# Kernel tuning notes

Measured on AMD Instinct MI355X. Metric: run time of the kernel, lower is better.

## Reference

```python
import jax, jax.numpy as jnp
import numpy as np

EPS = 1e-5
B, CIN, L = 512, 5, 1024   # batch, input channels, msp length == d_model
COUT, A, NB = 32, 13, 5    # CNN branch channels, max_atoms, num_bonds_prediction


def conv1d(x, w, pad, groups=1):
    # x: (N, C, L), w: (O, I/groups, K)
    return jax.lax.conv_general_dilated(
        x, w, window_strides=(1,), padding=[(pad, pad)],
        dimension_numbers=("NCH", "OIH", "NCH"), feature_group_count=groups)


def batchnorm(x, g, b):
    # training-mode BN over (N, L) per channel, as nn.BatchNorm1d in train()
    m = jnp.mean(x, axis=(0, 2), keepdims=True)
    v = jnp.var(x, axis=(0, 2), keepdims=True)
    return (x - m) * jax.lax.rsqrt(v + EPS) * g[None, :, None] + b[None, :, None]


def setup_inputs() -> dict:
    key = jax.random.key(0)
    ks = jax.random.split(key, 16)
    n = jax.random.normal
    inp = {
        "src": n(ks[0], (B, CIN, L), dtype=jnp.float32),
        "mask": jnp.ones((B, A), dtype=bool),
        "max_atoms": A,
        # CNN branch 1 (kernel 5) : depthwise, pointwise, BN, residual 1x1 conv
        "dw1": n(ks[1], (CIN, 1, 5), dtype=jnp.float32) * 0.2,
        "pw1": n(ks[2], (COUT, CIN, 1), dtype=jnp.float32) * 0.2,
        "g1": jnp.ones((COUT,), jnp.float32),
        "be1": jnp.zeros((COUT,), jnp.float32),
        "r1w": n(ks[3], (COUT, CIN, 1), dtype=jnp.float32) * 0.2,
        "r1b": jnp.zeros((COUT,), jnp.float32),
        # CNN branch 2 (kernel 3)
        "dw2": n(ks[4], (CIN, 1, 3), dtype=jnp.float32) * 0.2,
        "pw2": n(ks[5], (COUT, CIN, 1), dtype=jnp.float32) * 0.2,
        "g2": jnp.ones((COUT,), jnp.float32),
        "be2": jnp.zeros((COUT,), jnp.float32),
        "r2w": n(ks[6], (COUT, CIN, 1), dtype=jnp.float32) * 0.2,
        "r2b": jnp.zeros((COUT,), jnp.float32),
        # EdgeClassify2 linears: ll1 (2*COUT -> A), fl (2*L -> NB)
        "ll1w": n(ks[7], (A, 2 * COUT), dtype=jnp.float32) * 0.1,
        "ll1b": jnp.zeros((A,), jnp.float32),
        "flw": n(ks[8], (NB, 2 * L), dtype=jnp.float32) * 0.02,
        "flb": jnp.zeros((NB,), jnp.float32),
    }
    return inp


def reference(src, mask, max_atoms, dw1, pw1, g1, be1, r1w, r1b,
              dw2, pw2, g2, be2, r2w, r2b, ll1w, ll1b, flw, flb):
    # ---- CNN encoder ----
    e1 = jax.nn.relu(batchnorm(conv1d(conv1d(src, dw1, 2, groups=CIN), pw1, 0), g1, be1))
    e1 = e1 * (conv1d(src, r1w, 0) + r1b[None, :, None])
    e2 = jax.nn.relu(batchnorm(conv1d(conv1d(src, dw2, 1, groups=CIN), pw2, 0), g2, be2))
    e2 = e2 * (conv1d(src, r2w, 0) + r2b[None, :, None])
    x = jnp.concatenate([e1, e2], axis=1)          # (B, 2*COUT, L)
    # ---- EdgeClassify2 ----
    # ll1 over channel dim: (B, 2*COUT, L) -> (B, A, L)
    h = jnp.einsum("bcl,ac->bal", x, ll1w) + ll1b[None, :, None]
    # vectorized replacement of the O(A^2) python loop:
    # final_e[:, i, j] = concat(h[:, min(i,j)], h[:, max(i,j)])
    idx = jnp.arange(max_atoms)
    mn = jnp.minimum(idx[:, None], idx[None, :])   # (A, A)
    mx = jnp.maximum(idx[:, None], idx[None, :])
    final_e = jnp.concatenate([h[:, mn, :], h[:, mx, :]], axis=-1)  # (B, A, A, 2L)
    out = jnp.einsum("bijd,nd->bijn", final_e, flw) + flb           # (B, A, A, NB)
    return out
```

## Files before the change

### kernel.cpp

```cpp
#include <hip/hip_runtime.h>
#include <hip/hip_bf16.h>

#define BB 512
#define LL 1024
#define AA 13
#define NBP 5
#define NTOT (BB * LL)
#define EPSV 1e-5f

#define WS_MOM   0
#define WS_F     192
#define WS_CONST 256

template<int CTRL, int RM, bool BC>
__device__ __forceinline__ float dppadd(float v) {
    int t = __builtin_amdgcn_update_dpp(0, __float_as_int(v), CTRL, RM, 0xf, BC);
    return v + __int_as_float(t);
}
__device__ __forceinline__ float wave_sum(float v) {
    v = dppadd<0x111, 0xf, true >(v);
    v = dppadd<0x112, 0xf, true >(v);
    v = dppadd<0x114, 0xf, true >(v);
    v = dppadd<0x118, 0xf, true >(v);
    v = dppadd<0x142, 0xa, false>(v);
    v = dppadd<0x143, 0xc, false>(v);
    return v;
}

__global__ __launch_bounds__(256) void k_moments(
    const float* __restrict__ src,
    const float* __restrict__ dw1,
    const float* __restrict__ dw2,
    const float* __restrict__ flw,
    float* __restrict__ ws)
{
    __shared__ float red[4][40];
    __shared__ float fred[4];
    int tid = threadIdx.x;
    int gid = blockIdx.x * 256 + tid;
    int b = gid >> 7, L0 = (gid & 127) << 3;
    const float* sb = src + b * (5 * LL);

    float w1[5][5], w2[5][3];
#pragma unroll
    for (int c = 0; c < 5; c++) {
#pragma unroll
        for (int t = 0; t < 5; t++) w1[c][t] = dw1[c*5+t];
#pragma unroll
        for (int t = 0; t < 3; t++) w2[c][t] = dw2[c*3+t];
    }

    float x[5][16];
#pragma unroll
    for (int c5 = 0; c5 < 5; c5++) {
        const float* sp = sb + c5 * LL;
        float4 xa = (L0 >= 4)     ? *(const float4*)(sp + L0 - 4) : make_float4(0,0,0,0);
        float4 xb = *(const float4*)(sp + L0);
        float4 xc = *(const float4*)(sp + L0 + 4);
        float4 xd = (L0 <= 1012)  ? *(const float4*)(sp + L0 + 8) : make_float4(0,0,0,0);
        x[c5][0]=xa.x; x[c5][1]=xa.y; x[c5][2]=xa.z; x[c5][3]=xa.w;
        x[c5][4]=xb.x; x[c5][5]=xb.y; x[c5][6]=xb.z; x[c5][7]=xb.w;
        x[c5][8]=xc.x; x[c5][9]=xc.y; x[c5][10]=xc.z; x[c5][11]=xc.w;
        x[c5][12]=xd.x; x[c5][13]=xd.y; x[c5][14]=xd.z; x[c5][15]=xd.w;
    }

    float acc[40];
#pragma unroll
    for (int k = 0; k < 40; k++) acc[k] = 0.f;

#pragma unroll
    for (int k = 0; k < 8; k++) {
        float d1[5], d2[5];
#pragma unroll
        for (int c5 = 0; c5 < 5; c5++) {
            d1[c5] = w1[c5][0]*x[c5][k+2] + w1[c5][1]*x[c5][k+3] + w1[c5][2]*x[c5][k+4]
                   + w1[c5][3]*x[c5][k+5] + w1[c5][4]*x[c5][k+6];
            d2[c5] = w2[c5][0]*x[c5][k+3] + w2[c5][1]*x[c5][k+4] + w2[c5][2]*x[c5][k+5];
        }
#pragma unroll
        for (int j = 0; j < 5; j++) { acc[j] += d1[j]; acc[20+j] += d2[j]; }
#pragma unroll
        for (int j = 0; j < 5; j++)
#pragma unroll
            for (int kk = j; kk < 5; kk++) {
                int idx = j*(11-j)/2 + (kk - j);
                acc[5+idx]  += d1[j]*d1[kk];
                acc[25+idx] += d2[j]*d2[kk];
            }
    }

    int lane = tid & 63, wv = tid >> 6;
#pragma unroll
    for (int k = 0; k < 40; k++) acc[k] = wave_sum(acc[k]);
    if (lane == 63) {
#pragma unroll
        for (int k = 0; k < 40; k++) red[wv][k] = acc[k];
    }
    __syncthreads();
    if (tid < 40) {
        float v = red[0][tid] + red[1][tid] + red[2][tid] + red[3][tid];
        atomicAdd(&ws[WS_MOM + tid], v);
    }

    if (blockIdx.x < 10) {
        int nn = blockIdx.x;
        int n = nn < 5 ? nn : nn - 5;
        int off = nn < 5 ? 0 : LL;
        float4 v = *(const float4*)(flw + n * (2*LL) + off + tid * 4);
        float s = wave_sum(v.x + v.y + v.z + v.w);
        if (lane == 63) fred[wv] = s;
        __syncthreads();
        if (tid == 0) ws[WS_F + nn] = fred[0] + fred[1] + fred[2] + fred[3];
    }
}

__global__ __launch_bounds__(64) void k_prep(
    float* __restrict__ ws,
    const float* __restrict__ pw1, const float* __restrict__ pw2,
    const float* __restrict__ g1,  const float* __restrict__ be1,
    const float* __restrict__ g2,  const float* __restrict__ be2,
    const float* __restrict__ r1w, const float* __restrict__ r2w,
    const float* __restrict__ r1b, const float* __restrict__ r2b)
{
    int t = threadIdx.x;
    int br = t >> 5, o = t & 31;
    const float invN = 1.0f / (float)NTOT;
    const float* pw = br ? pw2 : pw1;
    const float* rw = br ? r2w : r1w;
    const float* s  = ws + WS_MOM + (br ? 20 : 0);
    const float* M  = ws + WS_MOM + (br ? 25 : 5);
    float pwv[5], rwv[5], md[5];
#pragma unroll
    for (int j = 0; j < 5; j++) { pwv[j] = pw[o*5+j]; rwv[j] = rw[o*5+j]; md[j] = s[j] * invN; }
    float meanY = 0.f;
#pragma unroll
    for (int j = 0; j < 5; j++) meanY += pwv[j] * md[j];
    float ey2 = 0.f;
#pragma unroll
    for (int j = 0; j < 5; j++)
#pragma unroll
        for (int k = 0; k < 5; k++) {
            int lo = j < k ? j : k, hi = j < k ? k : j;
            int idx = lo*(11-lo)/2 + (hi - lo);
            ey2 += pwv[j] * pwv[k] * (M[idx] * invN);
        }
    float varY = ey2 - meanY * meanY;
    if (varY < 0.f) varY = 0.f;
    float gg = br ? g2[o] : g1[o];
    float bb = br ? be2[o] : be1[o];
    float rb = br ? r2b[o] : r1b[o];
    float sc = gg * rsqrtf(varY + EPSV);
    float sh = bb - meanY * sc;

    float* dst = ws + WS_CONST + t * 16;
    dst[0] = pwv[0]*sc; dst[1] = pwv[1]*sc; dst[2] = pwv[2]*sc; dst[3] = pwv[3]*sc;
    dst[4] = pwv[4]*sc; dst[5] = sh;        dst[6] = rb;        dst[7] = 0.f;
    dst[8] = rwv[0];    dst[9] = rwv[1];    dst[10] = rwv[2];   dst[11] = rwv[3];
    dst[12] = rwv[4];   dst[13] = 0.f;      dst[14] = 0.f;      dst[15] = 0.f;
}

__global__ __launch_bounds__(512) void k_fused(
    const float* __restrict__ src,
    const float* __restrict__ dw1,
    const float* __restrict__ dw2,
    const float* __restrict__ flw,
    const float* __restrict__ ll1w,
    const float* __restrict__ ll1b,
    const float* __restrict__ flb,
    const float* __restrict__ ws,
    float* __restrict__ out)
{
    __shared__ __align__(16) float srcS[5][1040];
    __shared__ __align__(16) float SLds[64][12];
    __shared__ float llT[832];
    __shared__ float PQ[130];

    int tid = threadIdx.x, b = blockIdx.x;
    int lane = tid & 63;
    int gu = __builtin_amdgcn_readfirstlane(tid >> 6);
    int br = gu >> 2;

    const float* srcB = src + b * (5 * LL);

    for (int idx = tid; idx < 5 * 256; idx += 512) {
        int c5 = idx >> 8, q = idx & 255;
        float4 v = *(const float4*)(srcB + (c5 << 10) + (q << 2));
        *(float4*)&srcS[c5][(q << 2) + 8] = v;
    }
    if (tid < 5)       { srcS[tid][6] = 0.f; srcS[tid][7] = 0.f; }
    else if (tid < 10) { srcS[tid-5][1032] = 0.f; srcS[tid-5][1033] = 0.f; }
    for (int idx = tid; idx < 832; idx += 512) {
        int cc = idx / 13, a = idx - cc * 13;
        llT[idx] = ll1w[a * 64 + cc];
    }
    __syncthreads();

    float wdw[5][5];
    if (br == 0) {
#pragma unroll
        for (int c5 = 0; c5 < 5; c5++)
#pragma unroll
            for (int t = 0; t < 5; t++) wdw[c5][t] = dw1[c5*5+t];
    } else {
#pragma unroll
        for (int c5 = 0; c5 < 5; c5++) {
            wdw[c5][0] = 0.f; wdw[c5][1] = dw2[c5*3+0];
            wdw[c5][2] = dw2[c5*3+1]; wdw[c5][3] = dw2[c5*3+2]; wdw[c5][4] = 0.f;
        }
    }
    const float* cb = ws + WS_CONST + gu * 128;

    float acc[80];
#pragma unroll
    for (int k = 0; k < 80; k++) acc[k] = 0.f;

#pragma unroll 1
    for (int p = 0; p < 4; p++) {
        int l0 = (p << 8) + (lane << 2);
        float4 fw[10];
#pragma unroll
        for (int nn = 0; nn < 10; nn++) {
            int n = nn < 5 ? nn : nn - 5;
            int off = nn < 5 ? 0 : LL;
            fw[nn] = *(const float4*)(flw + n * (2*LL) + off + l0);
        }
        float dv[5][4], sv[5][4];
#pragma unroll
        for (int c5 = 0; c5 < 5; c5++) {
            int i0 = l0 + 8;
            float2 lh = *(const float2*)&srcS[c5][i0 - 2];
            float4 ct = *(const float4*)&srcS[c5][i0];
            float2 rh = *(const float2*)&srcS[c5][i0 + 4];
            float xx[8] = {lh.x, lh.y, ct.x, ct.y, ct.z, ct.w, rh.x, rh.y};
            sv[c5][0] = ct.x; sv[c5][1] = ct.y; sv[c5][2] = ct.z; sv[c5][3] = ct.w;
#pragma unroll
            for (int q = 0; q < 4; q++)
                dv[c5][q] = wdw[c5][0]*xx[q]   + wdw[c5][1]*xx[q+1] + wdw[c5][2]*xx[q+2]
                          + wdw[c5][3]*xx[q+3] + wdw[c5][4]*xx[q+4];
        }
#pragma unroll
        for (int ci = 0; ci < 8; ci++) {
            const float4 A  = *(const float4*)(cb + ci*16);
            const float4 B2 = *(const float4*)(cb + ci*16 + 4);
            const float4 R0 = *(const float4*)(cb + ci*16 + 8);
            const float4 R1 = *(const float4*)(cb + ci*16 + 12);
#pragma unroll
            for (int q = 0; q < 4; q++) {
                float y = B2.y + A.x*dv[0][q] + A.y*dv[1][q] + A.z*dv[2][q]
                                + A.w*dv[3][q] + B2.x*dv[4][q];
                float r = B2.z + R0.x*sv[0][q] + R0.y*sv[1][q] + R0.z*sv[2][q]
                                + R0.w*sv[3][q] + R1.x*sv[4][q];
                float e = fmaxf(y, 0.f) * r;
#pragma unroll
                for (int nn = 0; nn < 10; nn++) {
                    float f = (nn==0)?fw[0].x:(nn==1)?fw[1].x:(nn==2)?fw[2].x:(nn==3)?fw[3].x:
                              (nn==4)?fw[4].x:(nn==5)?fw[5].x:(nn==6)?fw[6].x:(nn==7)?fw[7].x:
                              (nn==8)?fw[8].x:fw[9].x;
                    float fq = (q==0) ? f :
                               (q==1) ? ((nn==0)?fw[0].y:(nn==1)?fw[1].y:(nn==2)?fw[2].y:(nn==3)?fw[3].y:
                                         (nn==4)?fw[4].y:(nn==5)?fw[5].y:(nn==6)?fw[6].y:(nn==7)?fw[7].y:
                                         (nn==8)?fw[8].y:fw[9].y) :
                               (q==2) ? ((nn==0)?fw[0].z:(nn==1)?fw[1].z:(nn==2)?fw[2].z:(nn==3)?fw[3].z:
                                         (nn==4)?fw[4].z:(nn==5)?fw[5].z:(nn==6)?fw[6].z:(nn==7)?fw[7].z:
                                         (nn==8)?fw[8].z:fw[9].z) :
                                        ((nn==0)?fw[0].w:(nn==1)?fw[1].w:(nn==2)?fw[2].w:(nn==3)?fw[3].w:
                                         (nn==4)?fw[4].w:(nn==5)?fw[5].w:(nn==6)?fw[6].w:(nn==7)?fw[7].w:
                                         (nn==8)?fw[8].w:fw[9].w);
                    acc[ci*10 + nn] += e * fq;
                }
            }
        }
    }

#pragma unroll
    for (int k = 0; k < 80; k++) acc[k] = wave_sum(acc[k]);
    if (lane == 63) {
#pragma unroll
        for (int ci = 0; ci < 8; ci++) {
            int c = gu * 8 + ci;
            *(float4*)&SLds[c][0] = make_float4(acc[ci*10+0], acc[ci*10+1], acc[ci*10+2], acc[ci*10+3]);
            *(float4*)&SLds[c][4] = make_float4(acc[ci*10+4], acc[ci*10+5], acc[ci*10+6], acc[ci*10+7]);
            *(float2*)&SLds[c][8] = make_float2(acc[ci*10+8], acc[ci*10+9]);
        }
    }
    __syncthreads();

    if (tid < 130) {
        int half = tid >= 65 ? 1 : 0;
        int q = tid - half * 65;
        int a = q / 5, n = q - a * 5;
        int col = half * 5 + n;
        float v = ll1b[a] * ws[WS_F + col];
#pragma unroll 8
        for (int cc = 0; cc < 64; cc++) v += llT[cc * 13 + a] * SLds[cc][col];
        PQ[tid] = v;
    }
    __syncthreads();

    for (int idx = tid; idx < AA * AA * NBP; idx += 512) {
        int i = idx / 65;
        int rr = idx - i * 65;
        int j = rr / 5, n = rr - j * 5;
        int mn = i < j ? i : j, mx = i < j ? j : i;
        out[b * (AA * AA * NBP) + idx] = PQ[mn * 5 + n] + PQ[65 + mx * 5 + n] + flb[n];
    }
}

extern "C" void kernel_launch(void* const* d_in, const int* in_sizes, int n_in,
                              void* d_out, int out_size, void* d_ws, size_t ws_size,
                              hipStream_t stream) {
    const float* src  = (const float*)d_in[0];
    const float* dw1  = (const float*)d_in[3];
    const float* pw1  = (const float*)d_in[4];
    const float* g1   = (const float*)d_in[5];
    const float* be1  = (const float*)d_in[6];
    const float* r1w  = (const float*)d_in[7];
    const float* r1b  = (const float*)d_in[8];
    const float* dw2  = (const float*)d_in[9];
    const float* pw2  = (const float*)d_in[10];
    const float* g2   = (const float*)d_in[11];
    const float* be2  = (const float*)d_in[12];
    const float* r2w  = (const float*)d_in[13];
    const float* r2b  = (const float*)d_in[14];
    const float* ll1w = (const float*)d_in[15];
    const float* ll1b = (const float*)d_in[16];
    const float* flw  = (const float*)d_in[17];
    const float* flb  = (const float*)d_in[18];
    float* ws  = (float*)d_ws;
    float* out = (float*)d_out;

    hipMemsetAsync(d_ws, 0, 1024, stream);
    k_moments<<<256, 256, 0, stream>>>(src, dw1, dw2, flw, ws);
    k_prep<<<1, 64, 0, stream>>>(ws, pw1, pw2, g1, be1, g2, be2, r1w, r2w, r1b, r2b);
    k_fused<<<BB, 512, 0, stream>>>(src, dw1, dw2, flw, ll1w, ll1b, flb, ws, out);
}
```

Baseline: 155.3 us.

## Fold BN prep into fused kernel, drop memset and atomics via per-block partials

Replaces atomic accumulation of BN moments with per-block partial writes, removing the workspace memset. The single-block prep kernel is eliminated; every fused block reduces the 256 partials and computes BN/pointwise constants itself into LDS. Also restructures the inner accumulation to reduce the 4 positions before the 10 projection updates, splits the depthwise conv by branch to skip zero taps, and sets launch bounds to hint occupancy. Costs redundant per-block reduction of partials and extra LDS.

Result: slower. 482.1 us (+210.4%).

```diff
diff --git a/kernel.cpp b/kernel.cpp
--- a/kernel.cpp
+++ b/kernel.cpp
@@ -8,9 +8,8 @@
 #define NTOT (BB * LL)
 #define EPSV 1e-5f
 
-#define WS_MOM   0
-#define WS_F     192
-#define WS_CONST 256
+#define WS_F    192
+#define WS_PART 256
 
 template<int CTRL, int RM, bool BC>
 __device__ __forceinline__ float dppadd(float v) {
@@ -54,10 +53,10 @@
 #pragma unroll
     for (int c5 = 0; c5 < 5; c5++) {
         const float* sp = sb + c5 * LL;
-        float4 xa = (L0 >= 4)     ? *(const float4*)(sp + L0 - 4) : make_float4(0,0,0,0);
+        float4 xa = (L0 >= 4)    ? *(const float4*)(sp + L0 - 4) : make_float4(0,0,0,0);
         float4 xb = *(const float4*)(sp + L0);
         float4 xc = *(const float4*)(sp + L0 + 4);
-        float4 xd = (L0 <= 1012)  ? *(const float4*)(sp + L0 + 8) : make_float4(0,0,0,0);
+        float4 xd = (L0 <= 1012) ? *(const float4*)(sp + L0 + 8) : make_float4(0,0,0,0);
         x[c5][0]=xa.x; x[c5][1]=xa.y; x[c5][2]=xa.z; x[c5][3]=xa.w;
         x[c5][4]=xb.x; x[c5][5]=xb.y; x[c5][6]=xb.z; x[c5][7]=xb.w;
         x[c5][8]=xc.x; x[c5][9]=xc.y; x[c5][10]=xc.z; x[c5][11]=xc.w;
@@ -98,8 +97,8 @@
     }
     __syncthreads();
     if (tid < 40) {
-        float v = red[0][tid] + red[1][tid] + red[2][tid] + red[3][tid];
-        atomicAdd(&ws[WS_MOM + tid], v);
+        ws[WS_PART + blockIdx.x * 40 + tid] =
+            red[0][tid] + red[1][tid] + red[2][tid] + red[3][tid];
     }
 
     if (blockIdx.x < 10) {
@@ -114,55 +113,15 @@
     }
 }
 
-__global__ __launch_bounds__(64) void k_prep(
-    float* __restrict__ ws,
+__global__ __launch_bounds__(512, 4) void k_fused(
+    const float* __restrict__ src,
+    const float* __restrict__ dw1,
+    const float* __restrict__ dw2,
     const float* __restrict__ pw1, const float* __restrict__ pw2,
     const float* __restrict__ g1,  const float* __restrict__ be1,
     const float* __restrict__ g2,  const float* __restrict__ be2,
     const float* __restrict__ r1w, const float* __restrict__ r2w,
-    const float* __restrict__ r1b, const float* __restrict__ r2b)
-{
-    int t = threadIdx.x;
-    int br = t >> 5, o = t & 31;
-    const float invN = 1.0f / (float)NTOT;
-    const float* pw = br ? pw2 : pw1;
-    const float* rw = br ? r2w : r1w;
-    const float* s  = ws + WS_MOM + (br ? 20 : 0);
-    const float* M  = ws + WS_MOM + (br ? 25 : 5);
-    float pwv[5], rwv[5], md[5];
-#pragma unroll
-    for (int j = 0; j < 5; j++) { pwv[j] = pw[o*5+j]; rwv[j] = rw[o*5+j]; md[j] = s[j] * invN; }
-    float meanY = 0.f;
-#pragma unroll
-    for (int j = 0; j < 5; j++) meanY += pwv[j] * md[j];
-    float ey2 = 0.f;
-#pragma unroll
-    for (int j = 0; j < 5; j++)
-#pragma unroll
-        for (int k = 0; k < 5; k++) {
-            int lo = j < k ? j : k, hi = j < k ? k : j;
-            int idx = lo*(11-lo)/2 + (hi - lo);
-            ey2 += pwv[j] * pwv[k] * (M[idx] * invN);
-        }
-    float varY = ey2 - meanY * meanY;
-    if (varY < 0.f) varY = 0.f;
-    float gg = br ? g2[o] : g1[o];
-    float bb = br ? be2[o] : be1[o];
-    float rb = br ? r2b[o] : r1b[o];
-    float sc = gg * rsqrtf(varY + EPSV);
-    float sh = bb - meanY * sc;
-
-    float* dst = ws + WS_CONST + t * 16;
-    dst[0] = pwv[0]*sc; dst[1] = pwv[1]*sc; dst[2] = pwv[2]*sc; dst[3] = pwv[3]*sc;
-    dst[4] = pwv[4]*sc; dst[5] = sh;        dst[6] = rb;        dst[7] = 0.f;
-    dst[8] = rwv[0];    dst[9] = rwv[1];    dst[10] = rwv[2];   dst[11] = rwv[3];
-    dst[12] = rwv[4];   dst[13] = 0.f;      dst[14] = 0.f;      dst[15] = 0.f;
-}
-
-__global__ __launch_bounds__(512) void k_fused(
-    const float* __restrict__ src,
-    const float* __restrict__ dw1,
-    const float* __restrict__ dw2,
+    const float* __restrict__ r1b, const float* __restrict__ r2b,
     const float* __restrict__ flw,
     const float* __restrict__ ll1w,
     const float* __restrict__ ll1b,
@@ -171,7 +130,9 @@
     float* __restrict__ out)
 {
     __shared__ __align__(16) float srcS[5][1040];
+    __shared__ __align__(16) float constS[64][16];
     __shared__ __align__(16) float SLds[64][12];
+    __shared__ float momS[40];
     __shared__ float llT[832];
     __shared__ float PQ[130];
 
@@ -187,12 +148,61 @@
         float4 v = *(const float4*)(srcB + (c5 << 10) + (q << 2));
         *(float4*)&srcS[c5][(q << 2) + 8] = v;
     }
-    if (tid < 5)       { srcS[tid][6] = 0.f; srcS[tid][7] = 0.f; }
-    else if (tid < 10) { srcS[tid-5][1032] = 0.f; srcS[tid-5][1033] = 0.f; }
+    if (tid < 40) {
+        int c5 = tid >> 3, j = tid & 7;
+        int i = (j < 4) ? (4 + j) : (1028 + j);
+        srcS[c5][i] = 0.f;
+    }
     for (int idx = tid; idx < 832; idx += 512) {
         int cc = idx / 13, a = idx - cc * 13;
         llT[idx] = ll1w[a * 64 + cc];
     }
+    if (tid < 320) {
+        int k = tid >> 3, sub = tid & 7;
+        float v = 0.f;
+#pragma unroll 8
+        for (int t2 = 0; t2 < 32; t2++) v += ws[WS_PART + (sub + (t2 << 3)) * 40 + k];
+        v += __shfl_xor(v, 1, 64);
+        v += __shfl_xor(v, 2, 64);
+        v += __shfl_xor(v, 4, 64);
+        if (sub == 0) momS[k] = v;
+    }
+    __syncthreads();
+    if (tid < 64) {
+        int brc = tid >> 5, o = tid & 31;
+        const float invN = 1.0f / (float)NTOT;
+        const float* pw = brc ? pw2 : pw1;
+        const float* rw = brc ? r2w : r1w;
+        const float* s  = momS + (brc ? 20 : 0);
+        const float* M  = momS + (brc ? 25 : 5);
+        float pwv[5], rwv[5], md[5];
+#pragma unroll
+        for (int j = 0; j < 5; j++) { pwv[j] = pw[o*5+j]; rwv[j] = rw[o*5+j]; md[j] = s[j] * invN; }
+        float meanY = 0.f;
+#pragma unroll
+        for (int j = 0; j < 5; j++) meanY += pwv[j] * md[j];
+        float ey2 = 0.f;
+#pragma unroll
+        for (int j = 0; j < 5; j++)
+#pragma unroll
+            for (int k = 0; k < 5; k++) {
+                int lo = j < k ? j : k, hi = j < k ? k : j;
+                int idx = lo*(11-lo)/2 + (hi - lo);
+                ey2 += pwv[j] * pwv[k] * (M[idx] * invN);
+            }
+        float varY = ey2 - meanY * meanY;
+        if (varY < 0.f) varY = 0.f;
+        float gg = brc ? g2[o] : g1[o];
+        float bb = brc ? be2[o] : be1[o];
+        float rb = brc ? r2b[o] : r1b[o];
+        float sc = gg * rsqrtf(varY + EPSV);
+        float sh = bb - meanY * sc;
+        float* dst = &constS[tid][0];
+        dst[0] = pwv[0]*sc; dst[1] = pwv[1]*sc; dst[2] = pwv[2]*sc; dst[3] = pwv[3]*sc;
+        dst[4] = pwv[4]*sc; dst[5] = sh;        dst[6] = rb;        dst[7] = 0.f;
+        dst[8] = rwv[0];    dst[9] = rwv[1];    dst[10] = rwv[2];   dst[11] = rwv[3];
+        dst[12] = rwv[4];   dst[13] = 0.f;      dst[14] = 0.f;      dst[15] = 0.f;
+    }
     __syncthreads();
 
     float wdw[5][5];
@@ -204,70 +214,67 @@
     } else {
 #pragma unroll
         for (int c5 = 0; c5 < 5; c5++) {
-            wdw[c5][0] = 0.f; wdw[c5][1] = dw2[c5*3+0];
-            wdw[c5][2] = dw2[c5*3+1]; wdw[c5][3] = dw2[c5*3+2]; wdw[c5][4] = 0.f;
-        }
-    }
-    const float* cb = ws + WS_CONST + gu * 128;
+            wdw[c5][0] = 0.f;
+            wdw[c5][1] = dw2[c5*3+0]; wdw[c5][2] = dw2[c5*3+1]; wdw[c5][3] = dw2[c5*3+2];
+            wdw[c5][4] = 0.f;
+        }
+    }
 
     float acc[80];
 #pragma unroll
     for (int k = 0; k < 80; k++) acc[k] = 0.f;
+    int c0 = gu << 3;
 
 #pragma unroll 1
     for (int p = 0; p < 4; p++) {
         int l0 = (p << 8) + (lane << 2);
-        float4 fw[10];
+        float fwv[10][4];
 #pragma unroll
         for (int nn = 0; nn < 10; nn++) {
             int n = nn < 5 ? nn : nn - 5;
             int off = nn < 5 ? 0 : LL;
-            fw[nn] = *(const float4*)(flw + n * (2*LL) + off + l0);
+            float4 t4 = *(const float4*)(flw + n * (2*LL) + off + l0);
+            fwv[nn][0] = t4.x; fwv[nn][1] = t4.y; fwv[nn][2] = t4.z; fwv[nn][3] = t4.w;
         }
         float dv[5][4], sv[5][4];
 #pragma unroll
         for (int c5 = 0; c5 < 5; c5++) {
             int i0 = l0 + 8;
-            float2 lh = *(const float2*)&srcS[c5][i0 - 2];
-            float4 ct = *(const float4*)&srcS[c5][i0];
-            float2 rh = *(const float2*)&srcS[c5][i0 + 4];
-            float xx[8] = {lh.x, lh.y, ct.x, ct.y, ct.z, ct.w, rh.x, rh.y};
-            sv[c5][0] = ct.x; sv[c5][1] = ct.y; sv[c5][2] = ct.z; sv[c5][3] = ct.w;
-#pragma unroll
-            for (int q = 0; q < 4; q++)
-                dv[c5][q] = wdw[c5][0]*xx[q]   + wdw[c5][1]*xx[q+1] + wdw[c5][2]*xx[q+2]
-                          + wdw[c5][3]*xx[q+3] + wdw[c5][4]*xx[q+4];
+            float4 xa = *(const float4*)&srcS[c5][i0 - 4];
+            float4 xb = *(const float4*)&srcS[c5][i0];
+            float4 xc = *(const float4*)&srcS[c5][i0 + 4];
+            float xx[12] = {xa.x, xa.y, xa.z, xa.w, xb.x, xb.y, xb.z, xb.w, xc.x, xc.y, xc.z, xc.w};
+            sv[c5][0] = xb.x; sv[c5][1] = xb.y; sv[c5][2] = xb.z; sv[c5][3] = xb.w;
+            if (br == 0) {
+#pragma unroll
+                for (int q = 0; q < 4; q++)
+                    dv[c5][q] = wdw[c5][0]*xx[q+2] + wdw[c5][1]*xx[q+3] + wdw[c5][2]*xx[q+4]
+                              + wdw[c5][3]*xx[q+5] + wdw[c5][4]*xx[q+6];
+            } else {
+#pragma unroll
+                for (int q = 0; q < 4; q++)
+                    dv[c5][q] = wdw[c5][1]*xx[q+3] + wdw[c5][2]*xx[q+4] + wdw[c5][3]*xx[q+5];
+            }
         }
 #pragma unroll
         for (int ci = 0; ci < 8; ci++) {
-            const float4 A  = *(const float4*)(cb + ci*16);
-            const float4 B2 = *(const float4*)(cb + ci*16 + 4);
-            const float4 R0 = *(const float4*)(cb + ci*16 + 8);
-            const float4 R1 = *(const float4*)(cb + ci*16 + 12);
+            const float4 A  = *(const float4*)&constS[c0+ci][0];
+            const float4 B2 = *(const float4*)&constS[c0+ci][4];
+            const float4 R0 = *(const float4*)&constS[c0+ci][8];
+            const float4 R1 = *(const float4*)&constS[c0+ci][12];
+            float e[4];
 #pragma unroll
             for (int q = 0; q < 4; q++) {
                 float y = B2.y + A.x*dv[0][q] + A.y*dv[1][q] + A.z*dv[2][q]
                                 + A.w*dv[3][q] + B2.x*dv[4][q];
                 float r = B2.z + R0.x*sv[0][q] + R0.y*sv[1][q] + R0.z*sv[2][q]
                                 + R0.w*sv[3][q] + R1.x*sv[4][q];
-                float e = fmaxf(y, 0.f) * r;
-#pragma unroll
-                for (int nn = 0; nn < 10; nn++) {
-                    float f = (nn==0)?fw[0].x:(nn==1)?fw[1].x:(nn==2)?fw[2].x:(nn==3)?fw[3].x:
-                              (nn==4)?fw[4].x:(nn==5)?fw[5].x:(nn==6)?fw[6].x:(nn==7)?fw[7].x:
-                              (nn==8)?fw[8].x:fw[9].x;
-                    float fq = (q==0) ? f :
-                               (q==1) ? ((nn==0)?fw[0].y:(nn==1)?fw[1].y:(nn==2)?fw[2].y:(nn==3)?fw[3].y:
-                                         (nn==4)?fw[4].y:(nn==5)?fw[5].y:(nn==6)?fw[6].y:(nn==7)?fw[7].y:
-                                         (nn==8)?fw[8].y:fw[9].y) :
-                               (q==2) ? ((nn==0)?fw[0].z:(nn==1)?fw[1].z:(nn==2)?fw[2].z:(nn==3)?fw[3].z:
-                                         (nn==4)?fw[4].z:(nn==5)?fw[5].z:(nn==6)?fw[6].z:(nn==7)?fw[7].z:
-                                         (nn==8)?fw[8].z:fw[9].z) :
-                                        ((nn==0)?fw[0].w:(nn==1)?fw[1].w:(nn==2)?fw[2].w:(nn==3)?fw[3].w:
-                                         (nn==4)?fw[4].w:(nn==5)?fw[5].w:(nn==6)?fw[6].w:(nn==7)?fw[7].w:
-                                         (nn==8)?fw[8].w:fw[9].w);
-                    acc[ci*10 + nn] += e * fq;
-                }
+                e[q] = fmaxf(y, 0.f) * r;
+            }
+#pragma unroll
+            for (int nn = 0; nn < 10; nn++) {
+                acc[ci*10 + nn] += e[0]*fwv[nn][0] + e[1]*fwv[nn][1]
+                                 + e[2]*fwv[nn][2] + e[3]*fwv[nn][3];
             }
         }
     }
@@ -277,7 +284,7 @@
     if (lane == 63) {
 #pragma unroll
         for (int ci = 0; ci < 8; ci++) {
-            int c = gu * 8 + ci;
+            int c = c0 + ci;
             *(float4*)&SLds[c][0] = make_float4(acc[ci*10+0], acc[ci*10+1], acc[ci*10+2], acc[ci*10+3]);
             *(float4*)&SLds[c][4] = make_float4(acc[ci*10+4], acc[ci*10+5], acc[ci*10+6], acc[ci*10+7]);
             *(float2*)&SLds[c][8] = make_float2(acc[ci*10+8], acc[ci*10+9]);
@@ -329,8 +336,7 @@
     float* ws  = (float*)d_ws;
     float* out = (float*)d_out;
 
-    hipMemsetAsync(d_ws, 0, 1024, stream);
     k_moments<<<256, 256, 0, stream>>>(src, dw1, dw2, flw, ws);
-    k_prep<<<1, 64, 0, stream>>>(ws, pw1, pw2, g1, be1, g2, be2, r1w, r2w, r1b, r2b);
-    k_fused<<<BB, 512, 0, stream>>>(src, dw1, dw2, flw, ll1w, ll1b, flb, ws, out);
-}
+    k_fused<<<BB, 512, 0, stream>>>(src, dw1, dw2, pw1, pw2, g1, be1, g2, be2,
+                                    r1w, r2w, r1b, r2b, flw, ll1w, ll1b, flb, ws, out);
+}
```
